# Kernel tuning notes

Measured on AMD Instinct MI355X. Metric: run time of the kernel, lower is better.

The kernel has to match this reference:

```python
import jax, jax.numpy as jnp
import numpy as np

DIM, DEPTH, DH, H, NLAT, MAXT, MAXF, FFM = 1024, 6, 64, 8, 64, 8, 16, 4
INNER = DH * H

def _ln(x, w, b, eps=1e-5):
    m = jnp.mean(x, axis=-1, keepdims=True)
    v = jnp.mean(jnp.square(x - m), axis=-1, keepdims=True)
    return (x - m) * jax.lax.rsqrt(v + eps) * w + b

def setup_inputs() -> dict:
    key = jax.random.key(0)
    ks = iter(jax.random.split(key, 32))
    s = 0.02
    d = {
        'x': jax.random.normal(next(ks), (2, 8, 16, 256, DIM), jnp.float32),
        'latents': jax.random.normal(next(ks), (NLAT, DIM), jnp.float32),
        'frame_emb': jax.random.normal(next(ks), (MAXF, DIM), jnp.float32),
        'media_emb': jax.random.normal(next(ks), (MAXT, 1, DIM), jnp.float32),
        'lnm_w': jnp.ones((DEPTH, DIM)), 'lnm_b': jnp.zeros((DEPTH, DIM)),
        'lnl_w': jnp.ones((DEPTH, DIM)), 'lnl_b': jnp.zeros((DEPTH, DIM)),
        'Wq': jax.random.normal(next(ks), (DEPTH, DIM, INNER), jnp.float32) * s,
        'Wkv': jax.random.normal(next(ks), (DEPTH, DIM, 2 * INNER), jnp.float32) * s,
        'Wo': jax.random.normal(next(ks), (DEPTH, INNER, DIM), jnp.float32) * s,
        'ffln_w': jnp.ones((DEPTH, DIM)), 'ffln_b': jnp.zeros((DEPTH, DIM)),
        'W1': jax.random.normal(next(ks), (DEPTH, DIM, FFM * DIM), jnp.float32) * s,
        'b1': jnp.zeros((DEPTH, FFM * DIM)),
        'W2': jax.random.normal(next(ks), (DEPTH, FFM * DIM, DIM), jnp.float32) * s,
        'b2': jnp.zeros((DEPTH, DIM)),
        'fln_w': jnp.ones((DIM,)), 'fln_b': jnp.zeros((DIM,)),
    }
    return d

def _split_heads(t):  # b T n (h d) -> b h T n d
    b, T, n, _ = t.shape
    return t.reshape(b, T, n, H, DH).transpose(0, 3, 1, 2, 4)

def _forward(x, latents, frame_emb, media_emb, lnm_w, lnm_b, lnl_w, lnl_b,
             Wq, Wkv, Wo, ffln_w, ffln_b, W1, b1, W2, b2, fln_w, fln_b):
    b, T, F, v, d = x.shape
    x = x + frame_emb[:F][None, None, :, None, :]      # b T F v d
    x = x.reshape(b, T, F * v, d)
    x = x + media_emb[:T]                              # [T,1,d] broadcasts
    lat = jnp.broadcast_to(latents, (b, T, NLAT, d))
    scale = DH ** -0.5
    for i in range(DEPTH):
        xn = _ln(x, lnm_w[i], lnm_b[i])
        ln_lat = _ln(lat, lnl_w[i], lnl_b[i])
        q = _split_heads(ln_lat @ Wq[i]) * scale       # b h T n2 dh
        kv = jnp.concatenate([xn, ln_lat], axis=2) @ Wkv[i]
        k, vv = jnp.split(kv, 2, axis=-1)
        k, vv = _split_heads(k), _split_heads(vv)      # b h T (n1+n2) dh
        sim = jnp.einsum('bhtid,bhtjd->bhtij', q, k)
        sim = sim - jax.lax.stop_gradient(jnp.max(sim, axis=-1, keepdims=True))
        attn = jax.nn.softmax(sim, axis=-1)
        o = jnp.einsum('bhtij,bhtjd->bhtid', attn, vv)
        o = o.transpose(0, 2, 3, 1, 4).reshape(b, T, NLAT, INNER)
        lat = (o @ Wo[i]) + lat
        h = _ln(lat, ffln_w[i], ffln_b[i])
        h = jax.nn.gelu(h @ W1[i] + b1[i], approximate=False) @ W2[i] + b2[i]
        lat = h + lat
    return _ln(lat, fln_w, fln_b)

def reference(x, latents, frame_emb, media_emb, lnm_w, lnm_b, lnl_w, lnl_b,
              Wq, Wkv, Wo, ffln_w, ffln_b, W1, b1, W2, b2, fln_w, fln_b):
    return _forward(x, latents, frame_emb, media_emb, lnm_w, lnm_b, lnl_w, lnl_b,
                    Wq, Wkv, Wo, ffln_w, ffln_b, W1, b1, W2, b2, fln_w, fln_b)
```

## Files before the change

kernel.cpp:

```cpp
#include <hip/hip_runtime.h>
#include <math.h>


#define DIM   1024
#define DEPTH 6
#define HEADS 8
#define NLAT  64
#define INNER 512
#define FFD   4096
#define XROWS 65536
#define LROWS 1024
#define NBT   16
#define QKVN  1536

typedef __attribute__((ext_vector_type(8))) short bf16x8;
typedef __attribute__((ext_vector_type(4))) float f32x4;

#define WAITV(n) asm volatile("s_waitcnt vmcnt(" #n ")" ::: "memory")

__device__ __forceinline__ short f2bf(float f) {
  union { float f; unsigned u; } v; v.f = f;
  unsigned r = v.u + 0x7fffu + ((v.u >> 16) & 1u);
  return (short)(r >> 16);
}

__device__ __forceinline__ void gload16(const void* g, void* l) {
  __builtin_amdgcn_global_load_lds(
      (const __attribute__((address_space(1))) unsigned int*)g,
      (__attribute__((address_space(3))) unsigned int*)l, 16, 0, 0);
}

__device__ __forceinline__ f32x4 zero_f4() { f32x4 z; z[0]=0.f; z[1]=0.f; z[2]=0.f; z[3]=0.f; return z; }
__device__ __forceinline__ bf16x8 zero_b8() { bf16x8 z;
#pragma unroll
  for (int e=0;e<8;e++) z[e]=0; return z; }

__global__ __launch_bounds__(256)
void prep_kernel(const float* __restrict__ x, const float* __restrict__ fe,
                 const float* __restrict__ me, short* __restrict__ xhat)
{
  int lane = threadIdx.x & 63;
  int r = blockIdx.x*4 + (threadIdx.x >> 6);
  int f = (r >> 8) & 15, tt = (r >> 12) & 7;
  const float4* xp = (const float4*)(x + (size_t)r*DIM);
  const float4* fp = (const float4*)(fe + (size_t)f*DIM);
  const float4* mp = (const float4*)(me + (size_t)tt*DIM);
  float y[16];
  float s = 0.f, sq = 0.f;
#pragma unroll
  for (int k = 0; k < 4; k++) {
    float4 xv = xp[k*64 + lane], fv = fp[k*64 + lane], mv = mp[k*64 + lane];
    float a0 = xv.x+fv.x+mv.x, a1 = xv.y+fv.y+mv.y, a2 = xv.z+fv.z+mv.z, a3 = xv.w+fv.w+mv.w;
    y[k*4+0]=a0; y[k*4+1]=a1; y[k*4+2]=a2; y[k*4+3]=a3;
    s += a0+a1+a2+a3; sq += a0*a0+a1*a1+a2*a2+a3*a3;
  }
#pragma unroll
  for (int off = 32; off >= 1; off >>= 1) {
    s  += __shfl_xor(s,  off, 64);
    sq += __shfl_xor(sq, off, 64);
  }
  float mean = s * (1.0f/DIM);
  float var  = sq * (1.0f/DIM) - mean*mean;
  float rs = rsqrtf(var + 1e-5f);
  short4* op = (short4*)(xhat + (size_t)r*DIM);
#pragma unroll
  for (int k = 0; k < 4; k++) {
    short4 o;
    o.x = f2bf((y[k*4+0]-mean)*rs); o.y = f2bf((y[k*4+1]-mean)*rs);
    o.z = f2bf((y[k*4+2]-mean)*rs); o.w = f2bf((y[k*4+3]-mean)*rs);
    op[k*64 + lane] = o;
  }
}

__device__ __forceinline__ void reduce2(float& s, float& sq, float* sh) {
#pragma unroll
  for (int off = 32; off >= 1; off >>= 1) {
    s  += __shfl_xor(s,  off, 64);
    sq += __shfl_xor(sq, off, 64);
  }
  int t = threadIdx.x;
  if ((t & 63) == 0) { sh[(t >> 6)*2] = s; sh[(t >> 6)*2 + 1] = sq; }
  __syncthreads();
  s  = sh[0] + sh[2] + sh[4] + sh[6];
  sq = sh[1] + sh[3] + sh[5] + sh[7];
}

__global__ __launch_bounds__(256)
void latinit_ln_kernel(const float* __restrict__ latents, const float* __restrict__ w,
                       const float* __restrict__ b, float* __restrict__ lat,
                       short* __restrict__ lnlat)
{
  __shared__ float sh[8];
  int r = blockIdx.x, t = threadIdx.x;
  int i = r & 63;
  float4 a = ((const float4*)(latents + (size_t)i*DIM))[t];
  ((float4*)(lat + (size_t)r*DIM))[t] = a;
  float s = a.x+a.y+a.z+a.w;
  float sq = a.x*a.x+a.y*a.y+a.z*a.z+a.w*a.w;
  reduce2(s, sq, sh);
  float mean = s*(1.0f/DIM), var = sq*(1.0f/DIM) - mean*mean;
  float rs = rsqrtf(var + 1e-5f);
  float4 wv = ((const float4*)w)[t], bv = ((const float4*)b)[t];
  short4 o;
  o.x = f2bf((a.x-mean)*rs*wv.x + bv.x);
  o.y = f2bf((a.y-mean)*rs*wv.y + bv.y);
  o.z = f2bf((a.z-mean)*rs*wv.z + bv.z);
  o.w = f2bf((a.w-mean)*rs*wv.w + bv.w);
  ((short4*)(lnlat + (size_t)r*DIM))[t] = o;
}

__global__ __launch_bounds__(256)
void kvbp_kernel(const float* __restrict__ lnm_b, const float* __restrict__ Wkv,
                 float* __restrict__ kvb_part)
{
  int z = blockIdx.x, i = blockIdx.y, t = threadIdx.x;
  const float* W = Wkv + (size_t)i*DIM*DIM;
  const float* bv = lnm_b + (size_t)i*DIM;
  float acc0=0,acc1=0,acc2=0,acc3=0;
  for (int k = z*64; k < z*64+64; k++) {
    float b = bv[k];
    const float* Wr = W + (size_t)k*DIM;
    acc0 += b * Wr[t];       acc1 += b * Wr[t+256];
    acc2 += b * Wr[t+512];   acc3 += b * Wr[t+768];
  }
  float* o = kvb_part + (size_t)(i*16 + z)*DIM;
  o[t] = acc0; o[t+256] = acc1; o[t+512] = acc2; o[t+768] = acc3;
}

__global__ __launch_bounds__(256)
void kvbred_kernel(const float* __restrict__ kvb_part, float* __restrict__ kvb)
{
  int i = blockIdx.x, t = threadIdx.x;
#pragma unroll
  for (int j = 0; j < 4; j++) {
    int col = t + j*256;
    float s = 0.f;
#pragma unroll
    for (int z = 0; z < 16; z++) s += kvb_part[(size_t)(i*16 + z)*DIM + col];
    kvb[i*DIM + col] = s;
  }
}

__global__ __launch_bounds__(256)
void tcast_all6_kernel(const float* __restrict__ Wkv, const float* __restrict__ Wq,
                       const float* __restrict__ Wo, const float* __restrict__ W1,
                       const float* __restrict__ W2, const float* __restrict__ lnm_w,
                       short* __restrict__ Wkvf_a, short* __restrict__ qkvW_a,
                       short* __restrict__ Wo_a, short* __restrict__ W1_a,
                       short* __restrict__ W2_a)
{
  int L = blockIdx.x / 2816;
  int b = blockIdx.x % 2816;
  const float* lWkv = Wkv + (size_t)L*DIM*DIM;
  const float* src; short* dst; const float* fold = nullptr; float scale = 1.0f;
  int K, N, bx, ntx;
  if (b < 256)      { src=lWkv; dst=Wkvf_a + (size_t)L*DIM*DIM; fold=lnm_w + (size_t)L*DIM; K=1024; N=1024; bx=b; ntx=16; }
  else if (b < 384) { src=Wq + (size_t)L*DIM*INNER; dst=qkvW_a + (size_t)L*QKVN*DIM; scale=0.125f; K=1024; N=512; bx=b-256; ntx=8; }
  else if (b < 640) { src=lWkv; dst=qkvW_a + (size_t)L*QKVN*DIM + (size_t)512*1024; K=1024; N=1024; bx=b-384; ntx=16; }
  else if (b < 768) { src=Wo + (size_t)L*INNER*DIM; dst=Wo_a + (size_t)L*INNER*DIM; K=512;  N=1024; bx=b-640; ntx=16; }
  else if (b < 1792){ src=W1 + (size_t)L*DIM*FFD; dst=W1_a + (size_t)L*DIM*FFD; K=1024; N=4096; bx=b-768; ntx=64; }
  else              { src=W2 + (size_t)L*FFD*DIM; dst=W2_a + (size_t)L*FFD*DIM; K=4096; N=1024; bx=b-1792; ntx=16; }
  int n0 = (bx % ntx)*64, k0 = (bx / ntx)*64;
  __shared__ float tile[64][65];
  int t = threadIdx.x;
#pragma unroll
  for (int i = 0; i < 16; i++) {
    int rr = (t >> 6) + i*4, cc = t & 63;
    float v = src[(size_t)(k0+rr)*N + n0 + cc] * scale;
    if (fold) v *= fold[k0 + rr];
    tile[rr][cc] = v;
  }
  __syncthreads();
#pragma unroll
  for (int i = 0; i < 16; i++) {
    int nn = (t >> 6) + i*4, kk = t & 63;
    dst[(size_t)(n0+nn)*K + k0 + kk] = f2bf(tile[kk][nn]);
  }
}

__global__ __launch_bounds__(512, 1)
void gemm256p_kernel(const short* __restrict__ A, const short* __restrict__ Bt,
                     short* __restrict__ C, const float* __restrict__ bias,
                     int M, int N, int K)
{
  __shared__ __align__(16) short lds[65536];
  char* ldsc = (char*)lds;
  const int t = threadIdx.x, lane = t & 63, wid = t >> 6;
  const int wm = wid >> 2, wn = wid & 3;

  const int nwg = gridDim.x * gridDim.y;
  const int id = blockIdx.y * gridDim.x + blockIdx.x;
  const int work = (id & 7) * (nwg >> 3) + (id >> 3);
  const int bn = work % gridDim.x, bm = work / gridDim.x;
  const int m0 = bm * 256, n0 = bn * 256;

  f32x4 acc[8][4];
#pragma unroll
  for (int m=0;m<8;m++)
#pragma unroll
    for (int n=0;n<4;n++) acc[m][n] = zero_f4();

  const int hK = K << 7;
  const short* pA[2]; const short* pB[2]; int ldst[2];
#pragma unroll
  for (int i = 0; i < 2; i++) {
    int chunk = i*512 + t;
    int rh = chunk >> 3, sl = chunk & 7;
    int ss = sl ^ (rh & 7);
    pA[i] = A + (size_t)(m0 + rh)*K + ss*8;
    pB[i] = Bt + (size_t)(n0 + rh)*K + ss*8;
    ldst[i] = (i*512 + (wid << 6))*16;
  }
  auto stage = [&](int tile, int mat, int half) {
    char* dbase = ldsc + mat*65536 + (tile & 1)*32768 + half*16384;
#pragma unroll
    for (int i = 0; i < 2; i++) {
      const short* src = (mat ? pB[i] : pA[i]) + half*hK + tile*64;
      gload16(src, dbase + ldst[i]);
    }
  };

  const int sk0 = (((lane >> 4)    ) ^ (lane & 7)) * 16;
  const int sk1 = ((4 + (lane >> 4)) ^ (lane & 7)) * 16;
  const int rowb = (lane & 15) * 128;
  const char* aB[2] = { ldsc + wm*16384 + rowb + sk0, ldsc + wm*16384 + rowb + sk1 };
  const char* bB[2] = { ldsc + 65536 + wn*8192 + rowb + sk0, ldsc + 65536 + wn*8192 + rowb + sk1 };

#define PHASE(BUF, Q, STAGE_STMT, GATE) do {                               \
    if ((Q) == 0) {                                                        \
      _Pragma("unroll") for (int n_=0;n_<4;n_++)                           \
        _Pragma("unroll") for (int k_=0;k_<2;k_++)                         \
          bfr[n_][k_] = *(const bf16x8*)(bB[k_] + (BUF)*32768 + n_*2048);  \
    }                                                                      \
    _Pragma("unroll") for (int i_=0;i_<2;i_++)                             \
      _Pragma("unroll") for (int k_=0;k_<2;k_++)                           \
        afr[i_][k_] = *(const bf16x8*)(aB[k_] + (BUF)*32768 + (2*(Q)+i_)*2048); \
    STAGE_STMT;                                                            \
    GATE;                                                                  \
    __builtin_amdgcn_sched_barrier(0);                                     \
    __builtin_amdgcn_s_barrier();                                          \
    asm volatile("s_waitcnt lgkmcnt(0)" ::: "memory");                     \
    __builtin_amdgcn_sched_barrier(0);                                     \
    __builtin_amdgcn_s_setprio(1);                                         \
    _Pragma("unroll") for (int k_=0;k_<2;k_++)                             \
      _Pragma("unroll") for (int i_=0;i_<2;i_++)                           \
        _Pragma("unroll") for (int n_=0;n_<4;n_++)                         \
          acc[2*(Q)+i_][n_] = __builtin_amdgcn_mfma_f32_16x16x32_bf16(     \
              afr[i_][k_], bfr[n_][k_], acc[2*(Q)+i_][n_], 0, 0, 0);       \
    __builtin_amdgcn_s_setprio(0);                                         \
    __builtin_amdgcn_sched_barrier(0);                                     \
    __builtin_amdgcn_s_barrier();                                          \
  } while (0)

  const int NU = K >> 7;
  stage(0, 0, 0); stage(0, 0, 1); stage(0, 1, 0); stage(0, 1, 1);
  stage(1, 1, 0); stage(1, 1, 1);
  WAITV(4);
  __builtin_amdgcn_sched_barrier(0);
  __builtin_amdgcn_s_barrier();

#pragma unroll 1
  for (int u = 0; u < NU; ++u) {
    const int t0 = 2*u, t1 = t0 + 1;
    const bool more = (u + 1 < NU);
    bf16x8 bfr[4][2], afr[2][2];
    PHASE(0, 0, stage(t1, 0, 0),               (void)0);
    PHASE(0, 1, stage(t1, 0, 1),               (void)0);
    PHASE(0, 2, if (more) stage(t0+2, 1, 0),   (void)0);
    PHASE(0, 3, if (more) stage(t0+2, 1, 1),   if (more) { WAITV(4); } else { WAITV(0); });
    PHASE(1, 0, if (more) stage(t0+2, 0, 0),   (void)0);
    PHASE(1, 1, if (more) stage(t0+2, 0, 1),   (void)0);
    PHASE(1, 2, if (more) stage(t1+2, 1, 0),   (void)0);
    PHASE(1, 3, if (more) stage(t1+2, 1, 1),   if (more) { WAITV(4); });
  }
#undef PHASE

  const int g = lane >> 4;
#pragma unroll
  for (int m=0;m<8;m++) {
#pragma unroll
    for (int n=0;n<4;n++) {
#pragma unroll
      for (int r=0;r<4;r++) {
        int mm = m0 + wm*128 + m*16 + g*4 + r;
        int nn = n0 + wn*64 + n*16 + (lane & 15);
        float v = acc[m][n][r] + bias[nn];
        C[(size_t)mm*N + nn] = f2bf(v);
      }
    }
  }
}

template<int EPI, bool HAS_BIAS>
__global__ __launch_bounds__(256, 2)
void gemm_kernel(const short* __restrict__ A, const short* __restrict__ Bt,
                 void* __restrict__ Cout, const float* __restrict__ bias,
                 int M, int N, int K, int ldk)
{
  __shared__ __align__(16) short As[128*64];
  __shared__ __align__(16) short Bs[128*64];
  const int t = threadIdx.x;
  const int lane = t & 63, w = t >> 6;
  const int m0 = blockIdx.x * 128, n0 = blockIdx.y * 128;
  const int wr = (w >> 1) * 64, wc = (w & 1) * 64;
  const short* Ap = A + (size_t)blockIdx.z * K;
  const short* Btp = Bt + (size_t)blockIdx.z * K;

  f32x4 acc[4][4];
#pragma unroll
  for (int i=0;i<4;i++)
#pragma unroll
    for (int j=0;j<4;j++) acc[i][j] = zero_f4();

  for (int kt = 0; kt < K; kt += 64) {
#pragma unroll
    for (int i = 0; i < 4; i++) {
      int chunk = i*256 + t;
      int row = chunk >> 3, slot = chunk & 7;
      int ss = slot ^ (row & 7);
      gload16(Ap + (size_t)(m0 + row)*ldk + kt + ss*8,
              (char*)As + (i*256 + (w<<6))*16);
    }
#pragma unroll
    for (int i = 0; i < 4; i++) {
      int chunk = i*256 + t;
      int row = chunk >> 3, slot = chunk & 7;
      int ss = slot ^ (row & 7);
      gload16(Btp + (size_t)(n0 + row)*ldk + kt + ss*8,
              (char*)Bs + (i*256 + (w<<6))*16);
    }
    __syncthreads();

#pragma unroll
    for (int ks = 0; ks < 2; ks++) {
      bf16x8 af[4], bfr[4];
#pragma unroll
      for (int i=0;i<4;i++) {
        int row = wr + i*16 + (lane & 15);
        int slot = (ks*4 + (lane >> 4)) ^ (row & 7);
        af[i] = *(const bf16x8*)((const char*)As + row*128 + slot*16);
        int nrow = wc + i*16 + (lane & 15);
        int nslot = (ks*4 + (lane >> 4)) ^ (nrow & 7);
        bfr[i] = *(const bf16x8*)((const char*)Bs + nrow*128 + nslot*16);
      }
#pragma unroll
      for (int i=0;i<4;i++)
#pragma unroll
        for (int j=0;j<4;j++)
          acc[i][j] = __builtin_amdgcn_mfma_f32_16x16x32_bf16(af[i], bfr[j], acc[i][j], 0, 0, 0);
    }
    __syncthreads();
  }

  const int g = lane >> 4;
#pragma unroll
  for (int i=0;i<4;i++) {
#pragma unroll
    for (int j=0;j<4;j++) {
#pragma unroll
      for (int r=0;r<4;r++) {
        int m = m0 + wr + i*16 + g*4 + r;
        int n = n0 + wc + j*16 + (lane & 15);
        float v = acc[i][j][r];
        if (EPI == 0) {
          if (HAS_BIAS) v += bias[n];
          ((short*)Cout)[(size_t)m*N + n] = f2bf(v);
        } else if (EPI == 1) {
          if (HAS_BIAS) v += bias[n];
          float gl = 0.5f * v * (1.0f + erff(v * 0.70710678f));
          ((short*)Cout)[(size_t)m*N + n] = f2bf(gl);
        } else {
          ((float*)Cout)[(size_t)blockIdx.z*M*N + (size_t)m*N + n] = v;
        }
      }
    }
  }
}

__global__ __launch_bounds__(256)
void wored_ffln_kernel(const float* __restrict__ part, float* __restrict__ lat,
                       const float* __restrict__ w, const float* __restrict__ bb,
                       short* __restrict__ hbuf)
{
  __shared__ float sh[8];
  int r = blockIdx.x, t = threadIdx.x;
  int idx = r*256 + t;
  float4 a = ((float4*)lat)[idx];
  float4 p0 = ((const float4*)part)[idx];
  float4 p1 = ((const float4*)(part + (size_t)LROWS*DIM))[idx];
  a.x += p0.x + p1.x; a.y += p0.y + p1.y; a.z += p0.z + p1.z; a.w += p0.w + p1.w;
  ((float4*)lat)[idx] = a;
  float s = a.x+a.y+a.z+a.w;
  float sq = a.x*a.x+a.y*a.y+a.z*a.z+a.w*a.w;
  reduce2(s, sq, sh);
  float mean = s*(1.0f/DIM), var = sq*(1.0f/DIM) - mean*mean;
  float rs = rsqrtf(var + 1e-5f);
  float4 wv = ((const float4*)w)[t], bv = ((const float4*)bb)[t];
  short4 o;
  o.x = f2bf((a.x-mean)*rs*wv.x + bv.x);
  o.y = f2bf((a.y-mean)*rs*wv.y + bv.y);
  o.z = f2bf((a.z-mean)*rs*wv.z + bv.z);
  o.w = f2bf((a.w-mean)*rs*wv.w + bv.w);
  ((short4*)(hbuf + (size_t)r*DIM))[t] = o;
}

template<bool LAST>
__global__ __launch_bounds__(256)
void w2red_ln_kernel(const float* __restrict__ part, const float* __restrict__ b2,
                     float* __restrict__ lat, const float* __restrict__ w,
                     const float* __restrict__ bb, void* __restrict__ dst)
{
  __shared__ float sh[8];
  int r = blockIdx.x, t = threadIdx.x;
  int idx = r*256 + t;
  float4 a = ((float4*)lat)[idx];
  float4 b4 = ((const float4*)b2)[t];
  a.x += b4.x; a.y += b4.y; a.z += b4.z; a.w += b4.w;
#pragma unroll
  for (int z = 0; z < 4; z++) {
    float4 p = ((const float4*)(part + (size_t)z*LROWS*DIM))[idx];
    a.x += p.x; a.y += p.y; a.z += p.z; a.w += p.w;
  }
  ((float4*)lat)[idx] = a;
  float s = a.x+a.y+a.z+a.w;
  float sq = a.x*a.x+a.y*a.y+a.z*a.z+a.w*a.w;
  reduce2(s, sq, sh);
  float mean = s*(1.0f/DIM), var = sq*(1.0f/DIM) - mean*mean;
  float rs = rsqrtf(var + 1e-5f);
  float4 wv = ((const float4*)w)[t], bv = ((const float4*)bb)[t];
  float o0 = (a.x-mean)*rs*wv.x + bv.x;
  float o1 = (a.y-mean)*rs*wv.y + bv.y;
  float o2 = (a.z-mean)*rs*wv.z + bv.z;
  float o3 = (a.w-mean)*rs*wv.w + bv.w;
  if (LAST) {
    float4 o; o.x=o0; o.y=o1; o.z=o2; o.w=o3;
    ((float4*)((float*)dst + (size_t)r*DIM))[t] = o;
  } else {
    short4 o; o.x=f2bf(o0); o.y=f2bf(o1); o.z=f2bf(o2); o.w=f2bf(o3);
    ((short4*)((short*)dst + (size_t)r*DIM))[t] = o;
  }
}

__global__ __launch_bounds__(256, 2)
void attn_part_kernel(const short* __restrict__ qkvlat, const short* __restrict__ kvbuf,
                      float* __restrict__ part_O, float* __restrict__ part_m,
                      float* __restrict__ part_l)
{
  __shared__ __align__(16) short q_sh[64*64];
  __shared__ __align__(16) short K_sh[128*64];
  __shared__ __align__(16) short VT_sh[64*128];
  __shared__ __align__(16) short P_sh[64*132];

  const int t = threadIdx.x, lane = t & 63, w = t >> 6;
  const int bid = blockIdx.x;
  const int s = bid & 3, bh = bid >> 2;
  const int h = bh & 7, bt = bh >> 3;

  {
    const short* qsrc = qkvlat + (size_t)(bt*64)*QKVN + h*64;
#pragma unroll
    for (int i = 0; i < 2; i++) {
      int chunk = i*256 + t;
      int row = chunk >> 3, slot = chunk & 7;
      gload16(qsrc + (size_t)row*QKVN + ((slot ^ (row & 7))*8),
              (char*)q_sh + (i*256 + (w<<6))*16);
    }
  }

  float m_run[4], l_run[4];
#pragma unroll
  for (int r=0;r<4;r++){ m_run[r] = -1e30f; l_run[r] = 0.f; }
  f32x4 oacc[4];
#pragma unroll
  for (int j=0;j<4;j++) oacc[j] = zero_f4();

  const int nch = (s == 3) ? 9 : 8;
  for (int c5 = 0; c5 < nch; c5++) {
    __syncthreads();
    const bool isLat = (c5 == 8);
    const int jv = isLat ? 4 : 8;
    const short* kbase; int kstride, valid;
    if (!isLat) {
      kbase = kvbuf + ((size_t)bt*4096 + (s*8 + c5)*128)*DIM + h*64;
      kstride = DIM; valid = 128;
    } else {
      kbase = qkvlat + (size_t)(bt*64)*QKVN + 512 + h*64;
      kstride = QKVN; valid = 64;
    }
    const short* vbase = kbase + 512;

#pragma unroll
    for (int i = 0; i < 4; i++) {
      int chunk = i*256 + t;
      int row = chunk >> 3, slot = chunk & 7;
      gload16(kbase + (size_t)row*kstride + ((slot ^ (row & 7))*8),
              (char*)K_sh + (i*256 + (w<<6))*16);
    }
#pragma unroll
    for (int i = 0; i < 4; i++) {
      int c = i*256 + t;
      int row = c >> 3, slot = c & 7;
      bf16x8 v = (row < valid) ? *(const bf16x8*)(vbase + (size_t)row*kstride + slot*8) : zero_b8();
#pragma unroll
      for (int e=0;e<8;e++) {
        int dh = slot*8 + e;
        VT_sh[dh*128 + ((row + (dh & 0x78)) & 127)] = v[e];
      }
    }
    __syncthreads();

    f32x4 sacc[8];
#pragma unroll
    for (int j=0;j<8;j++) sacc[j] = zero_f4();
#pragma unroll
    for (int ks=0; ks<2; ks++) {
      int arow = w*16 + (lane & 15);
      int aslot = (ks*4 + (lane >> 4)) ^ (arow & 7);
      bf16x8 af = *(const bf16x8*)((const char*)q_sh + arow*128 + aslot*16);
#pragma unroll
      for (int j=0;j<8;j++) {
        int brow = j*16 + (lane & 15);
        int bslot = (ks*4 + (lane >> 4)) ^ (brow & 7);
        bf16x8 bv = *(const bf16x8*)((const char*)K_sh + brow*128 + bslot*16);
        sacc[j] = __builtin_amdgcn_mfma_f32_16x16x32_bf16(af, bv, sacc[j], 0, 0, 0);
      }
    }

    float mx[4];
#pragma unroll
    for (int r=0;r<4;r++) mx[r] = -1e30f;
#pragma unroll
    for (int j=0;j<8;j++) {
      if (j < jv) {
#pragma unroll
        for (int r=0;r<4;r++) mx[r] = fmaxf(mx[r], sacc[j][r]);
      }
    }
#pragma unroll
    for (int m2=1; m2<16; m2<<=1) {
#pragma unroll
      for (int r=0;r<4;r++) mx[r] = fmaxf(mx[r], __shfl_xor(mx[r], m2, 64));
    }
    float alpha[4], rowsum[4];
#pragma unroll
    for (int r=0;r<4;r++) {
      float nm = fmaxf(m_run[r], mx[r]);
      alpha[r] = __expf(m_run[r] - nm);
      m_run[r] = nm;
      rowsum[r] = 0.f;
    }
#pragma unroll
    for (int j=0;j<8;j++) {
#pragma unroll
      for (int r=0;r<4;r++) {
        float p = 0.f;
        if (j < jv) { p = __expf(sacc[j][r] - m_run[r]); rowsum[r] += p; }
        P_sh[(w*16 + (lane>>4)*4 + r)*132 + j*16 + (lane & 15)] = f2bf(p);
      }
    }
#pragma unroll
    for (int m2=1; m2<16; m2<<=1) {
#pragma unroll
      for (int r=0;r<4;r++) rowsum[r] += __shfl_xor(rowsum[r], m2, 64);
    }
#pragma unroll
    for (int r=0;r<4;r++) l_run[r] = l_run[r]*alpha[r] + rowsum[r];
#pragma unroll
    for (int j=0;j<4;j++) {
#pragma unroll
      for (int r=0;r<4;r++) oacc[j][r] *= alpha[r];
    }
    __syncthreads();

#pragma unroll
    for (int ks=0; ks<4; ks++) {
      int prow = w*16 + (lane & 15);
      bf16x8 af = *(const bf16x8*)((const char*)P_sh + prow*264 + ks*64 + (lane >> 4)*16);
#pragma unroll
      for (int j=0;j<4;j++) {
        int dh = j*16 + (lane & 15);
        int kb = (ks*4 + (lane >> 4))*8;
        const short* vp = VT_sh + dh*128 + ((kb + (dh & 0x78)) & 127);
        bf16x8 bv = *(const bf16x8*)vp;
        oacc[j] = __builtin_amdgcn_mfma_f32_16x16x32_bf16(af, bv, oacc[j], 0, 0, 0);
      }
    }
  }

  {
    float* Ob = part_O + (size_t)bid*4096;
    int rbase = w*16 + (lane>>4)*4;
#pragma unroll
    for (int j=0;j<4;j++) {
#pragma unroll
      for (int r=0;r<4;r++)
        Ob[(rbase + r)*64 + j*16 + (lane & 15)] = oacc[j][r];
    }
    if ((lane & 15) == 0) {
#pragma unroll
      for (int r=0;r<4;r++) {
        part_m[(size_t)bid*64 + rbase + r] = m_run[r];
        part_l[(size_t)bid*64 + rbase + r] = l_run[r];
      }
    }
  }
}

__global__ __launch_bounds__(256)
void attn_combine_kernel(const float* __restrict__ part_O, const float* __restrict__ part_m,
                         const float* __restrict__ part_l, short* __restrict__ obuf)
{
  int bh = blockIdx.x, t = threadIdx.x;
  int q = t >> 2, c0 = (t & 3) * 16;
  int bt = bh >> 3, h = bh & 7;
  float m4[4], w4[4];
  float mmax = -1e30f;
#pragma unroll
  for (int s=0;s<4;s++) { m4[s] = part_m[(size_t)(bh*4+s)*64 + q]; mmax = fmaxf(mmax, m4[s]); }
  float lt = 0.f;
#pragma unroll
  for (int s=0;s<4;s++) { w4[s] = __expf(m4[s] - mmax); lt += w4[s] * part_l[(size_t)(bh*4+s)*64 + q]; }
  float inv = 1.0f / lt;
  float4 acc[4];
#pragma unroll
  for (int u=0;u<4;u++) { acc[u].x=0.f; acc[u].y=0.f; acc[u].z=0.f; acc[u].w=0.f; }
#pragma unroll
  for (int s=0;s<4;s++) {
    const float4* Ob = (const float4*)(part_O + ((size_t)(bh*4+s)*64 + q)*64 + c0);
#pragma unroll
    for (int u=0;u<4;u++) {
      float4 v = Ob[u];
      acc[u].x += w4[s]*v.x; acc[u].y += w4[s]*v.y;
      acc[u].z += w4[s]*v.z; acc[u].w += w4[s]*v.w;
    }
  }
  short* ob = obuf + (size_t)(bt*64 + q)*INNER + h*64 + c0;
#pragma unroll
  for (int u=0;u<4;u++) {
    short4 o;
    o.x = f2bf(acc[u].x*inv); o.y = f2bf(acc[u].y*inv);
    o.z = f2bf(acc[u].z*inv); o.w = f2bf(acc[u].w*inv);
    ((short4*)ob)[u] = o;
  }
}

extern "C" void kernel_launch(void* const* d_in, const int* in_sizes, int n_in,
                              void* d_out, int out_size, void* d_ws, size_t ws_size,
                              hipStream_t stream)
{
  (void)in_sizes; (void)n_in; (void)out_size; (void)ws_size;
  const float* x        = (const float*)d_in[0];
  const float* latents  = (const float*)d_in[1];
  const float* frame_e  = (const float*)d_in[2];
  const float* media_e  = (const float*)d_in[3];
  const float* lnm_w    = (const float*)d_in[4];
  const float* lnm_b    = (const float*)d_in[5];
  const float* lnl_w    = (const float*)d_in[6];
  const float* lnl_b    = (const float*)d_in[7];
  const float* Wq       = (const float*)d_in[8];
  const float* Wkv      = (const float*)d_in[9];
  const float* Wo       = (const float*)d_in[10];
  const float* ffln_w   = (const float*)d_in[11];
  const float* ffln_b   = (const float*)d_in[12];
  const float* W1       = (const float*)d_in[13];
  const float* b1       = (const float*)d_in[14];
  const float* W2       = (const float*)d_in[15];
  const float* b2       = (const float*)d_in[16];
  const float* fln_w    = (const float*)d_in[17];
  const float* fln_b    = (const float*)d_in[18];
  float* out = (float*)d_out;

  char* ws = (char*)d_ws;
  size_t off = 0;
  short* xhat   = (short*)(ws + off); off += (size_t)XROWS*DIM*2;
  short* kvbuf  = (short*)(ws + off); off += (size_t)XROWS*DIM*2;
  short* Wkvf_a = (short*)(ws + off); off += (size_t)DEPTH*DIM*DIM*2;
  short* qkvW_a = (short*)(ws + off); off += (size_t)DEPTH*QKVN*DIM*2;
  short* Wo_a   = (short*)(ws + off); off += (size_t)DEPTH*INNER*DIM*2;
  short* W1_a   = (short*)(ws + off); off += (size_t)DEPTH*DIM*FFD*2;
  short* W2_a   = (short*)(ws + off); off += (size_t)DEPTH*FFD*DIM*2;
  float* kvb    = (float*)(ws + off); off += (size_t)DEPTH*DIM*4;
  float* kvbp   = (float*)(ws + off); off += (size_t)DEPTH*16*DIM*4;
  float* lat    = (float*)(ws + off); off += (size_t)LROWS*DIM*4;
  short* lnlat  = (short*)(ws + off); off += (size_t)LROWS*DIM*2;
  short* qkvlat = (short*)(ws + off); off += (size_t)LROWS*QKVN*2;
  short* obuf   = (short*)(ws + off); off += (size_t)LROWS*INNER*2;
  short* hbuf   = (short*)(ws + off); off += (size_t)LROWS*DIM*2;
  short* h1     = (short*)(ws + off); off += (size_t)LROWS*FFD*2;
  float* wopart = (float*)(ws + off); off += (size_t)2*LROWS*DIM*4;
  float* part_O = (float*)(ws + off); off += (size_t)4*LROWS*DIM*4;
  float* w2part = part_O;
  float* part_m = (float*)(ws + off); off += (size_t)512*64*4;
  float* part_l = (float*)(ws + off); off += (size_t)512*64*4;

  prep_kernel<<<XROWS/4, 256, 0, stream>>>(x, frame_e, media_e, xhat);
  latinit_ln_kernel<<<LROWS, 256, 0, stream>>>(latents, lnl_w, lnl_b, lat, lnlat);
  kvbp_kernel<<<dim3(16, DEPTH), 256, 0, stream>>>(lnm_b, Wkv, kvbp);
  kvbred_kernel<<<DEPTH, 256, 0, stream>>>(kvbp, kvb);
  tcast_all6_kernel<<<DEPTH*2816, 256, 0, stream>>>(
      Wkv, Wq, Wo, W1, W2, lnm_w, Wkvf_a, qkvW_a, Wo_a, W1_a, W2_a);

  for (int i = 0; i < DEPTH; i++) {
    const short* Wkv_f = Wkvf_a + (size_t)i*DIM*DIM;
    const short* qkvW  = qkvW_a + (size_t)i*QKVN*DIM;
    const short* Wo_h  = Wo_a   + (size_t)i*INNER*DIM;
    const short* W1_h  = W1_a   + (size_t)i*DIM*FFD;
    const short* W2_h  = W2_a   + (size_t)i*FFD*DIM;

    gemm_kernel<0,false><<<dim3(LROWS/128, QKVN/128), 256, 0, stream>>>(
        lnlat, qkvW, qkvlat, nullptr, LROWS, QKVN, DIM, DIM);
    gemm256p_kernel<<<dim3(DIM/256, XROWS/256), 512, 0, stream>>>(
        xhat, Wkv_f, kvbuf, kvb + i*DIM, XROWS, DIM, DIM);
    attn_part_kernel<<<512, 256, 0, stream>>>(qkvlat, kvbuf, part_O, part_m, part_l);
    attn_combine_kernel<<<128, 256, 0, stream>>>(part_O, part_m, part_l, obuf);
    gemm_kernel<4,false><<<dim3(LROWS/128, DIM/128, 2), 256, 0, stream>>>(
        obuf, Wo_h, wopart, nullptr, LROWS, DIM, 256, INNER);
    wored_ffln_kernel<<<LROWS, 256, 0, stream>>>(
        wopart, lat, ffln_w + i*DIM, ffln_b + i*DIM, hbuf);
    gemm_kernel<1,true><<<dim3(LROWS/128, FFD/128), 256, 0, stream>>>(
        hbuf, W1_h, h1, b1 + (size_t)i*FFD, LROWS, FFD, DIM, DIM);
    gemm_kernel<4,false><<<dim3(LROWS/128, DIM/128, 4), 256, 0, stream>>>(
        h1, W2_h, w2part, nullptr, LROWS, DIM, DIM, FFD);
    if (i < DEPTH-1)
      w2red_ln_kernel<false><<<LROWS, 256, 0, stream>>>(
          w2part, b2 + (size_t)i*DIM, lat, lnl_w + (i+1)*DIM, lnl_b + (i+1)*DIM, lnlat);
    else
      w2red_ln_kernel<true><<<LROWS, 256, 0, stream>>>(
          w2part, b2 + (size_t)i*DIM, lat, fln_w, fln_b, out);
  }
}
```

Measured before the change: 1.925 ms.

## Merge prep kernels and fuse QKV with KV GEMM into single launches

Folds the input prep, latent init, weight transpose-cast and KV-bias partial kernels into one block-indexed launch. It also merges the small latent QKV GEMM with the large KV GEMM into one kernel, so the 96 QKV tiles run beside the 1024 KV tiles. The Wo GEMM split-K goes from 2 to 4 with a 4-way partial reduction. This removes launch gaps and tail idle time, at the cost of a larger shared-memory footprint for the QKV blocks and more partial-sum traffic for Wo.

```diff
diff --git a/kernel.cpp b/kernel.cpp
--- a/kernel.cpp
+++ b/kernel.cpp
@@ -35,44 +35,7 @@
 #pragma unroll
   for (int e=0;e<8;e++) z[e]=0; return z; }
 
-__global__ __launch_bounds__(256)
-void prep_kernel(const float* __restrict__ x, const float* __restrict__ fe,
-                 const float* __restrict__ me, short* __restrict__ xhat)
-{
-  int lane = threadIdx.x & 63;
-  int r = blockIdx.x*4 + (threadIdx.x >> 6);
-  int f = (r >> 8) & 15, tt = (r >> 12) & 7;
-  const float4* xp = (const float4*)(x + (size_t)r*DIM);
-  const float4* fp = (const float4*)(fe + (size_t)f*DIM);
-  const float4* mp = (const float4*)(me + (size_t)tt*DIM);
-  float y[16];
-  float s = 0.f, sq = 0.f;
-#pragma unroll
-  for (int k = 0; k < 4; k++) {
-    float4 xv = xp[k*64 + lane], fv = fp[k*64 + lane], mv = mp[k*64 + lane];
-    float a0 = xv.x+fv.x+mv.x, a1 = xv.y+fv.y+mv.y, a2 = xv.z+fv.z+mv.z, a3 = xv.w+fv.w+mv.w;
-    y[k*4+0]=a0; y[k*4+1]=a1; y[k*4+2]=a2; y[k*4+3]=a3;
-    s += a0+a1+a2+a3; sq += a0*a0+a1*a1+a2*a2+a3*a3;
-  }
-#pragma unroll
-  for (int off = 32; off >= 1; off >>= 1) {
-    s  += __shfl_xor(s,  off, 64);
-    sq += __shfl_xor(sq, off, 64);
-  }
-  float mean = s * (1.0f/DIM);
-  float var  = sq * (1.0f/DIM) - mean*mean;
-  float rs = rsqrtf(var + 1e-5f);
-  short4* op = (short4*)(xhat + (size_t)r*DIM);
-#pragma unroll
-  for (int k = 0; k < 4; k++) {
-    short4 o;
-    o.x = f2bf((y[k*4+0]-mean)*rs); o.y = f2bf((y[k*4+1]-mean)*rs);
-    o.z = f2bf((y[k*4+2]-mean)*rs); o.w = f2bf((y[k*4+3]-mean)*rs);
-    op[k*64 + lane] = o;
-  }
-}
-
-__device__ __forceinline__ void reduce2(float& s, float& sq, float* sh) {
+__device__ __forceinline__ void reduce2s(float& s, float& sq, float* sh) {
 #pragma unroll
   for (int off = 32; off >= 1; off >>= 1) {
     s  += __shfl_xor(s,  off, 64);
@@ -86,45 +49,113 @@
 }
 
 __global__ __launch_bounds__(256)
-void latinit_ln_kernel(const float* __restrict__ latents, const float* __restrict__ w,
-                       const float* __restrict__ b, float* __restrict__ lat,
-                       short* __restrict__ lnlat)
-{
-  __shared__ float sh[8];
-  int r = blockIdx.x, t = threadIdx.x;
-  int i = r & 63;
-  float4 a = ((const float4*)(latents + (size_t)i*DIM))[t];
-  ((float4*)(lat + (size_t)r*DIM))[t] = a;
-  float s = a.x+a.y+a.z+a.w;
-  float sq = a.x*a.x+a.y*a.y+a.z*a.z+a.w*a.w;
-  reduce2(s, sq, sh);
-  float mean = s*(1.0f/DIM), var = sq*(1.0f/DIM) - mean*mean;
-  float rs = rsqrtf(var + 1e-5f);
-  float4 wv = ((const float4*)w)[t], bv = ((const float4*)b)[t];
-  short4 o;
-  o.x = f2bf((a.x-mean)*rs*wv.x + bv.x);
-  o.y = f2bf((a.y-mean)*rs*wv.y + bv.y);
-  o.z = f2bf((a.z-mean)*rs*wv.z + bv.z);
-  o.w = f2bf((a.w-mean)*rs*wv.w + bv.w);
-  ((short4*)(lnlat + (size_t)r*DIM))[t] = o;
-}
-
-__global__ __launch_bounds__(256)
-void kvbp_kernel(const float* __restrict__ lnm_b, const float* __restrict__ Wkv,
-                 float* __restrict__ kvb_part)
-{
-  int z = blockIdx.x, i = blockIdx.y, t = threadIdx.x;
-  const float* W = Wkv + (size_t)i*DIM*DIM;
-  const float* bv = lnm_b + (size_t)i*DIM;
-  float acc0=0,acc1=0,acc2=0,acc3=0;
-  for (int k = z*64; k < z*64+64; k++) {
-    float b = bv[k];
-    const float* Wr = W + (size_t)k*DIM;
-    acc0 += b * Wr[t];       acc1 += b * Wr[t+256];
-    acc2 += b * Wr[t+512];   acc3 += b * Wr[t+768];
-  }
-  float* o = kvb_part + (size_t)(i*16 + z)*DIM;
-  o[t] = acc0; o[t+256] = acc1; o[t+512] = acc2; o[t+768] = acc3;
+void mega0_kernel(const float* __restrict__ x, const float* __restrict__ fe,
+                  const float* __restrict__ me, short* __restrict__ xhat,
+                  const float* __restrict__ latents, const float* __restrict__ lnl_w,
+                  const float* __restrict__ lnl_b, float* __restrict__ lat,
+                  short* __restrict__ lnlat,
+                  const float* __restrict__ Wkv, const float* __restrict__ Wq,
+                  const float* __restrict__ Wo, const float* __restrict__ W1,
+                  const float* __restrict__ W2, const float* __restrict__ lnm_w,
+                  short* __restrict__ Wkvf_a, short* __restrict__ qkvW_a,
+                  short* __restrict__ Wo_a, short* __restrict__ W1_a,
+                  short* __restrict__ W2_a,
+                  const float* __restrict__ lnm_b, float* __restrict__ kvb_part)
+{
+  __shared__ float smem[64*65];
+  const int blk = blockIdx.x, t = threadIdx.x;
+
+  if (blk < 16384) {
+    int lane = t & 63;
+    int r = blk*4 + (t >> 6);
+    int f = (r >> 8) & 15, tt = (r >> 12) & 7;
+    const float4* xp = (const float4*)(x + (size_t)r*DIM);
+    const float4* fp = (const float4*)(fe + (size_t)f*DIM);
+    const float4* mp = (const float4*)(me + (size_t)tt*DIM);
+    float y[16];
+    float s = 0.f, sq = 0.f;
+#pragma unroll
+    for (int k = 0; k < 4; k++) {
+      float4 xv = xp[k*64 + lane], fv = fp[k*64 + lane], mv = mp[k*64 + lane];
+      float a0 = xv.x+fv.x+mv.x, a1 = xv.y+fv.y+mv.y, a2 = xv.z+fv.z+mv.z, a3 = xv.w+fv.w+mv.w;
+      y[k*4+0]=a0; y[k*4+1]=a1; y[k*4+2]=a2; y[k*4+3]=a3;
+      s += a0+a1+a2+a3; sq += a0*a0+a1*a1+a2*a2+a3*a3;
+    }
+#pragma unroll
+    for (int off = 32; off >= 1; off >>= 1) {
+      s  += __shfl_xor(s,  off, 64);
+      sq += __shfl_xor(sq, off, 64);
+    }
+    float mean = s * (1.0f/DIM);
+    float var  = sq * (1.0f/DIM) - mean*mean;
+    float rs = rsqrtf(var + 1e-5f);
+    short4* op = (short4*)(xhat + (size_t)r*DIM);
+#pragma unroll
+    for (int k = 0; k < 4; k++) {
+      short4 o;
+      o.x = f2bf((y[k*4+0]-mean)*rs); o.y = f2bf((y[k*4+1]-mean)*rs);
+      o.z = f2bf((y[k*4+2]-mean)*rs); o.w = f2bf((y[k*4+3]-mean)*rs);
+      op[k*64 + lane] = o;
+    }
+  } else if (blk < 17408) {
+    int r = blk - 16384;
+    int i = r & 63;
+    float4 a = ((const float4*)(latents + (size_t)i*DIM))[t];
+    ((float4*)(lat + (size_t)r*DIM))[t] = a;
+    float s = a.x+a.y+a.z+a.w;
+    float sq = a.x*a.x+a.y*a.y+a.z*a.z+a.w*a.w;
+    reduce2s(s, sq, smem);
+    float mean = s*(1.0f/DIM), var = sq*(1.0f/DIM) - mean*mean;
+    float rs = rsqrtf(var + 1e-5f);
+    float4 wv = ((const float4*)lnl_w)[t], bv = ((const float4*)lnl_b)[t];
+    short4 o;
+    o.x = f2bf((a.x-mean)*rs*wv.x + bv.x);
+    o.y = f2bf((a.y-mean)*rs*wv.y + bv.y);
+    o.z = f2bf((a.z-mean)*rs*wv.z + bv.z);
+    o.w = f2bf((a.w-mean)*rs*wv.w + bv.w);
+    ((short4*)(lnlat + (size_t)r*DIM))[t] = o;
+  } else if (blk < 34304) {
+    int bb = blk - 17408;
+    int L = bb / 2816;
+    int b = bb % 2816;
+    const float* lWkv = Wkv + (size_t)L*DIM*DIM;
+    const float* src; short* dst; const float* fold = nullptr; float scale = 1.0f;
+    int K, N, bx, ntx;
+    if (b < 256)      { src=lWkv; dst=Wkvf_a + (size_t)L*DIM*DIM; fold=lnm_w + (size_t)L*DIM; K=1024; N=1024; bx=b; ntx=16; }
+    else if (b < 384) { src=Wq + (size_t)L*DIM*INNER; dst=qkvW_a + (size_t)L*QKVN*DIM; scale=0.125f; K=1024; N=512; bx=b-256; ntx=8; }
+    else if (b < 640) { src=lWkv; dst=qkvW_a + (size_t)L*QKVN*DIM + (size_t)512*1024; K=1024; N=1024; bx=b-384; ntx=16; }
+    else if (b < 768) { src=Wo + (size_t)L*INNER*DIM; dst=Wo_a + (size_t)L*INNER*DIM; K=512;  N=1024; bx=b-640; ntx=16; }
+    else if (b < 1792){ src=W1 + (size_t)L*DIM*FFD; dst=W1_a + (size_t)L*DIM*FFD; K=1024; N=4096; bx=b-768; ntx=64; }
+    else              { src=W2 + (size_t)L*FFD*DIM; dst=W2_a + (size_t)L*FFD*DIM; K=4096; N=1024; bx=b-1792; ntx=16; }
+    int n0 = (bx % ntx)*64, k0 = (bx / ntx)*64;
+#pragma unroll
+    for (int i = 0; i < 16; i++) {
+      int rr = (t >> 6) + i*4, cc = t & 63;
+      float v = src[(size_t)(k0+rr)*N + n0 + cc] * scale;
+      if (fold) v *= fold[k0 + rr];
+      smem[rr*65 + cc] = v;
+    }
+    __syncthreads();
+#pragma unroll
+    for (int i = 0; i < 16; i++) {
+      int nn = (t >> 6) + i*4, kk = t & 63;
+      dst[(size_t)(n0+nn)*K + k0 + kk] = f2bf(smem[kk*65 + nn]);
+    }
+  } else {
+    int b2 = blk - 34304;
+    int z = b2 & 15, i = b2 >> 4;
+    const float* W = Wkv + (size_t)i*DIM*DIM;
+    const float* bv = lnm_b + (size_t)i*DIM;
+    float acc0=0,acc1=0,acc2=0,acc3=0;
+    for (int k = z*64; k < z*64+64; k++) {
+      float b3 = bv[k];
+      const float* Wr = W + (size_t)k*DIM;
+      acc0 += b3 * Wr[t];       acc1 += b3 * Wr[t+256];
+      acc2 += b3 * Wr[t+512];   acc3 += b3 * Wr[t+768];
+    }
+    float* o = kvb_part + (size_t)(i*16 + z)*DIM;
+    o[t] = acc0; o[t+256] = acc1; o[t+512] = acc2; o[t+768] = acc3;
+  }
 }
 
 __global__ __launch_bounds__(256)
@@ -141,57 +172,17 @@
   }
 }
 
-__global__ __launch_bounds__(256)
-void tcast_all6_kernel(const float* __restrict__ Wkv, const float* __restrict__ Wq,
-                       const float* __restrict__ Wo, const float* __restrict__ W1,
-                       const float* __restrict__ W2, const float* __restrict__ lnm_w,
-                       short* __restrict__ Wkvf_a, short* __restrict__ qkvW_a,
-                       short* __restrict__ Wo_a, short* __restrict__ W1_a,
-                       short* __restrict__ W2_a)
-{
-  int L = blockIdx.x / 2816;
-  int b = blockIdx.x % 2816;
-  const float* lWkv = Wkv + (size_t)L*DIM*DIM;
-  const float* src; short* dst; const float* fold = nullptr; float scale = 1.0f;
-  int K, N, bx, ntx;
-  if (b < 256)      { src=lWkv; dst=Wkvf_a + (size_t)L*DIM*DIM; fold=lnm_w + (size_t)L*DIM; K=1024; N=1024; bx=b; ntx=16; }
-  else if (b < 384) { src=Wq + (size_t)L*DIM*INNER; dst=qkvW_a + (size_t)L*QKVN*DIM; scale=0.125f; K=1024; N=512; bx=b-256; ntx=8; }
-  else if (b < 640) { src=lWkv; dst=qkvW_a + (size_t)L*QKVN*DIM + (size_t)512*1024; K=1024; N=1024; bx=b-384; ntx=16; }
-  else if (b < 768) { src=Wo + (size_t)L*INNER*DIM; dst=Wo_a + (size_t)L*INNER*DIM; K=512;  N=1024; bx=b-640; ntx=16; }
-  else if (b < 1792){ src=W1 + (size_t)L*DIM*FFD; dst=W1_a + (size_t)L*DIM*FFD; K=1024; N=4096; bx=b-768; ntx=64; }
-  else              { src=W2 + (size_t)L*FFD*DIM; dst=W2_a + (size_t)L*FFD*DIM; K=4096; N=1024; bx=b-1792; ntx=16; }
-  int n0 = (bx % ntx)*64, k0 = (bx / ntx)*64;
-  __shared__ float tile[64][65];
-  int t = threadIdx.x;
-#pragma unroll
-  for (int i = 0; i < 16; i++) {
-    int rr = (t >> 6) + i*4, cc = t & 63;
-    float v = src[(size_t)(k0+rr)*N + n0 + cc] * scale;
-    if (fold) v *= fold[k0 + rr];
-    tile[rr][cc] = v;
-  }
-  __syncthreads();
-#pragma unroll
-  for (int i = 0; i < 16; i++) {
-    int nn = (t >> 6) + i*4, kk = t & 63;
-    dst[(size_t)(n0+nn)*K + k0 + kk] = f2bf(tile[kk][nn]);
-  }
-}
-
-__global__ __launch_bounds__(512, 1)
-void gemm256p_kernel(const short* __restrict__ A, const short* __restrict__ Bt,
-                     short* __restrict__ C, const float* __restrict__ bias,
-                     int M, int N, int K)
-{
-  __shared__ __align__(16) short lds[65536];
-  char* ldsc = (char*)lds;
+
+__device__ __forceinline__ void kv256_path(
+    const short* __restrict__ A, const short* __restrict__ Bt,
+    short* __restrict__ C, const float* __restrict__ bias, int id, char* ldsc)
+{
   const int t = threadIdx.x, lane = t & 63, wid = t >> 6;
   const int wm = wid >> 2, wn = wid & 3;
-
-  const int nwg = gridDim.x * gridDim.y;
-  const int id = blockIdx.y * gridDim.x + blockIdx.x;
-  const int work = (id & 7) * (nwg >> 3) + (id >> 3);
-  const int bn = work % gridDim.x, bm = work / gridDim.x;
+  const int K = DIM, N = DIM;
+
+  const int work = (id & 7) * 128 + (id >> 3);
+  const int bn = work & 3, bm = work >> 2;
   const int m0 = bm * 256, n0 = bn * 256;
 
   f32x4 acc[8][4];
@@ -291,6 +282,89 @@
   }
 }
 
+__device__ __forceinline__ void qkv_path(
+    const short* __restrict__ A, const short* __restrict__ Bt,
+    short* __restrict__ C, int q, char* ldsc)
+{
+  const int t = threadIdx.x, lane = t & 63, wid = t >> 6;
+  const int m0 = (q & 7) * 128, n0 = (q >> 3) * 128;
+  const int wr = (wid >> 2) * 64, wc = (wid & 3) * 32;
+  char* As = ldsc;
+  char* Bs = ldsc + 16384;
+
+  f32x4 acc[4][2];
+#pragma unroll
+  for (int i=0;i<4;i++)
+#pragma unroll
+    for (int j=0;j<2;j++) acc[i][j] = zero_f4();
+
+  for (int kt = 0; kt < DIM; kt += 64) {
+#pragma unroll
+    for (int i = 0; i < 2; i++) {
+      int chunk = i*512 + t;
+      int row = chunk >> 3, slot = chunk & 7;
+      int ss = slot ^ (row & 7);
+      gload16(A + (size_t)(m0 + row)*DIM + kt + ss*8, As + (i*512 + (wid<<6))*16);
+    }
+#pragma unroll
+    for (int i = 0; i < 2; i++) {
+      int chunk = i*512 + t;
+      int row = chunk >> 3, slot = chunk & 7;
+      int ss = slot ^ (row & 7);
+      gload16(Bt + (size_t)(n0 + row)*DIM + kt + ss*8, Bs + (i*512 + (wid<<6))*16);
+    }
+    __syncthreads();
+#pragma unroll
+    for (int ks = 0; ks < 2; ks++) {
+      bf16x8 af[4], bfr[2];
+#pragma unroll
+      for (int i=0;i<4;i++) {
+        int row = wr + i*16 + (lane & 15);
+        int slot = (ks*4 + (lane >> 4)) ^ (row & 7);
+        af[i] = *(const bf16x8*)(As + row*128 + slot*16);
+      }
+#pragma unroll
+      for (int j=0;j<2;j++) {
+        int row = wc + j*16 + (lane & 15);
+        int slot = (ks*4 + (lane >> 4)) ^ (row & 7);
+        bfr[j] = *(const bf16x8*)(Bs + row*128 + slot*16);
+      }
+#pragma unroll
+      for (int i=0;i<4;i++)
+#pragma unroll
+        for (int j=0;j<2;j++)
+          acc[i][j] = __builtin_amdgcn_mfma_f32_16x16x32_bf16(af[i], bfr[j], acc[i][j], 0, 0, 0);
+    }
+    __syncthreads();
+  }
+
+  const int g = lane >> 4;
+#pragma unroll
+  for (int i=0;i<4;i++) {
+#pragma unroll
+    for (int j=0;j<2;j++) {
+#pragma unroll
+      for (int r=0;r<4;r++) {
+        int mm = m0 + wr + i*16 + g*4 + r;
+        int nn = n0 + wc + j*16 + (lane & 15);
+        C[(size_t)mm*QKVN + nn] = f2bf(acc[i][j][r]);
+      }
+    }
+  }
+}
+
+__global__ __launch_bounds__(512, 1)
+void mega1_kernel(const short* __restrict__ xhat, const short* __restrict__ Wkvf,
+                  const float* __restrict__ kvb_i, short* __restrict__ kvbuf,
+                  const short* __restrict__ lnlat, const short* __restrict__ qkvW,
+                  short* __restrict__ qkvlat)
+{
+  __shared__ __align__(16) short lds[65536];
+  int b = blockIdx.x;
+  if (b < 1024) kv256_path(xhat, Wkvf, kvbuf, kvb_i, b, (char*)lds);
+  else          qkv_path(lnlat, qkvW, qkvlat, b - 1024, (char*)lds);
+}
+
 template<int EPI, bool HAS_BIAS>
 __global__ __launch_bounds__(256, 2)
 void gemm_kernel(const short* __restrict__ A, const short* __restrict__ Bt,
@@ -362,10 +436,7 @@
         int m = m0 + wr + i*16 + g*4 + r;
         int n = n0 + wc + j*16 + (lane & 15);
         float v = acc[i][j][r];
-        if (EPI == 0) {
-          if (HAS_BIAS) v += bias[n];
-          ((short*)Cout)[(size_t)m*N + n] = f2bf(v);
-        } else if (EPI == 1) {
+        if (EPI == 1) {
           if (HAS_BIAS) v += bias[n];
           float gl = 0.5f * v * (1.0f + erff(v * 0.70710678f));
           ((short*)Cout)[(size_t)m*N + n] = f2bf(gl);
@@ -386,13 +457,15 @@
   int r = blockIdx.x, t = threadIdx.x;
   int idx = r*256 + t;
   float4 a = ((float4*)lat)[idx];
-  float4 p0 = ((const float4*)part)[idx];
-  float4 p1 = ((const float4*)(part + (size_t)LROWS*DIM))[idx];
-  a.x += p0.x + p1.x; a.y += p0.y + p1.y; a.z += p0.z + p1.z; a.w += p0.w + p1.w;
+#pragma unroll
+  for (int z = 0; z < 4; z++) {
+    float4 p = ((const float4*)(part + (size_t)z*LROWS*DIM))[idx];
+    a.x += p.x; a.y += p.y; a.z += p.z; a.w += p.w;
+  }
   ((float4*)lat)[idx] = a;
   float s = a.x+a.y+a.z+a.w;
   float sq = a.x*a.x+a.y*a.y+a.z*a.z+a.w*a.w;
-  reduce2(s, sq, sh);
+  reduce2s(s, sq, sh);
   float mean = s*(1.0f/DIM), var = sq*(1.0f/DIM) - mean*mean;
   float rs = rsqrtf(var + 1e-5f);
   float4 wv = ((const float4*)w)[t], bv = ((const float4*)bb)[t];
@@ -424,7 +497,7 @@
   ((float4*)lat)[idx] = a;
   float s = a.x+a.y+a.z+a.w;
   float sq = a.x*a.x+a.y*a.y+a.z*a.z+a.w*a.w;
-  reduce2(s, sq, sh);
+  reduce2s(s, sq, sh);
   float mean = s*(1.0f/DIM), var = sq*(1.0f/DIM) - mean*mean;
   float rs = rsqrtf(var + 1e-5f);
   float4 wv = ((const float4*)w)[t], bv = ((const float4*)bb)[t];
@@ -687,18 +760,19 @@
   short* obuf   = (short*)(ws + off); off += (size_t)LROWS*INNER*2;
   short* hbuf   = (short*)(ws + off); off += (size_t)LROWS*DIM*2;
   short* h1     = (short*)(ws + off); off += (size_t)LROWS*FFD*2;
-  float* wopart = (float*)(ws + off); off += (size_t)2*LROWS*DIM*4;
+  float* wopart = (float*)(ws + off); off += (size_t)4*LROWS*DIM*4;
   float* part_O = (float*)(ws + off); off += (size_t)4*LROWS*DIM*4;
   float* w2part = part_O;
   float* part_m = (float*)(ws + off); off += (size_t)512*64*4;
   float* part_l = (float*)(ws + off); off += (size_t)512*64*4;
 
-  prep_kernel<<<XROWS/4, 256, 0, stream>>>(x, frame_e, media_e, xhat);
-  latinit_ln_kernel<<<LROWS, 256, 0, stream>>>(latents, lnl_w, lnl_b, lat, lnlat);
-  kvbp_kernel<<<dim3(16, DEPTH), 256, 0, stream>>>(lnm_b, Wkv, kvbp);
+  mega0_kernel<<<34400, 256, 0, stream>>>(
+      x, frame_e, media_e, xhat,
+      latents, lnl_w, lnl_b, lat, lnlat,
+      Wkv, Wq, Wo, W1, W2, lnm_w,
+      Wkvf_a, qkvW_a, Wo_a, W1_a, W2_a,
+      lnm_b, kvbp);
   kvbred_kernel<<<DEPTH, 256, 0, stream>>>(kvbp, kvb);
-  tcast_all6_kernel<<<DEPTH*2816, 256, 0, stream>>>(
-      Wkv, Wq, Wo, W1, W2, lnm_w, Wkvf_a, qkvW_a, Wo_a, W1_a, W2_a);
 
   for (int i = 0; i < DEPTH; i++) {
     const short* Wkv_f = Wkvf_a + (size_t)i*DIM*DIM;
@@ -707,14 +781,12 @@
     const short* W1_h  = W1_a   + (size_t)i*DIM*FFD;
     const short* W2_h  = W2_a   + (size_t)i*FFD*DIM;
 
-    gemm_kernel<0,false><<<dim3(LROWS/128, QKVN/128), 256, 0, stream>>>(
-        lnlat, qkvW, qkvlat, nullptr, LROWS, QKVN, DIM, DIM);
-    gemm256p_kernel<<<dim3(DIM/256, XROWS/256), 512, 0, stream>>>(
-        xhat, Wkv_f, kvbuf, kvb + i*DIM, XROWS, DIM, DIM);
+    mega1_kernel<<<1120, 512, 0, stream>>>(
+        xhat, Wkv_f, kvb + i*DIM, kvbuf, lnlat, qkvW, qkvlat);
     attn_part_kernel<<<512, 256, 0, stream>>>(qkvlat, kvbuf, part_O, part_m, part_l);
     attn_combine_kernel<<<128, 256, 0, stream>>>(part_O, part_m, part_l, obuf);
-    gemm_kernel<4,false><<<dim3(LROWS/128, DIM/128, 2), 256, 0, stream>>>(
-        obuf, Wo_h, wopart, nullptr, LROWS, DIM, 256, INNER);
+    gemm_kernel<4,false><<<dim3(LROWS/128, DIM/128, 4), 256, 0, stream>>>(
+        obuf, Wo_h, wopart, nullptr, LROWS, DIM, 128, INNER);
     wored_ffln_kernel<<<LROWS, 256, 0, stream>>>(
         wopart, lat, ffln_w + i*DIM, ffln_b + i*DIM, hbuf);
     gemm_kernel<1,true><<<dim3(LROWS/128, FFD/128), 256, 0, stream>>>(
```

Result: no change. 1.892 ms (-1.7%).
